# Kernel tuning notes

Hardware: AMD Instinct MI355X
Metric: run time of the kernel (lower is better)

## Reference

```python
import jax, jax.numpy as jnp
import numpy as np

D, D_SEQ, D_HEAD, N_HEAD = 256, 1280, 48, 8
N_NODE, B_GRAPH, S_LEN = 2048, 8, 1024
HDH = N_HEAD * D_HEAD  # 384
SCALE = float(np.sqrt(D_HEAD))
LN_EPS = 1e-5


def setup_inputs() -> dict:
    key = jax.random.key(0)
    ks = jax.random.split(key, 12)
    node = jax.random.normal(ks[0], (N_NODE, D), dtype=jnp.float32)
    emb = jax.random.normal(ks[1], (B_GRAPH, S_LEN, D_SEQ), dtype=jnp.float32)
    mask = jax.random.randint(ks[2], (B_GRAPH, S_LEN), 0, 2, dtype=jnp.int32)
    batch = jnp.sort(jax.random.randint(ks[3], (N_NODE,), 0, B_GRAPH, dtype=jnp.int64))
    def lin(k, fan_in, fan_out):
        lim = 1.0 / np.sqrt(fan_in)
        return jax.random.uniform(k, (fan_in, fan_out), jnp.float32, -lim, lim)
    return {
        "node": node,
        "packed_sequence_emb": emb,
        "packed_sequence_mask": mask,
        "batch": batch,
        "ln_g": jnp.ones((D,), jnp.float32),
        "ln_b": jnp.zeros((D,), jnp.float32),
        "Wq": lin(ks[4], D, HDH),
        "Wk": lin(ks[5], D_SEQ, HDH),
        "Wv": lin(ks[6], D_SEQ, HDH),
        "Wg": lin(ks[7], D, HDH),
        "bg": jnp.zeros((HDH,), jnp.float32),
        "Wback": lin(ks[8], HDH, D),
        "bback": jnp.zeros((D,), jnp.float32),
    }


def _layernorm(x, g, b):
    mu = jnp.mean(x, axis=-1, keepdims=True)
    var = jnp.mean(jnp.square(x - mu), axis=-1, keepdims=True)
    return (x - mu) * jax.lax.rsqrt(var + LN_EPS) * g + b


def reference(node, packed_sequence_emb, packed_sequence_mask, batch,
              ln_g, ln_b, Wq, Wk, Wv, Wg, bg, Wback, bback):
    N = node.shape[0]
    y = _layernorm(node, ln_g, ln_b)                                   # [N, D]
    q = (y @ Wq).reshape(N, N_HEAD, D_HEAD)                            # [N, H, Dh]
    k = (packed_sequence_emb @ Wk).reshape(B_GRAPH, S_LEN, N_HEAD, D_HEAD)
    v = (packed_sequence_emb @ Wv).reshape(B_GRAPH, S_LEN, N_HEAD, D_HEAD)

    # scores[n, s, h] = <q[n,h], k[batch[n], s, h]> / sqrt(Dh)
    scores_all = jnp.einsum('nhd,bshd->nbsh', q, k) / SCALE            # [N, B, S, H]
    scores = jnp.take_along_axis(
        scores_all, batch[:, None, None, None].astype(jnp.int32), axis=1
    )[:, 0]                                                            # [N, S, H]

    # masked softmax over sequence axis (dim=1), mask broadcast over heads
    mask_f = packed_sequence_mask[batch].astype(scores.dtype)[:, :, None]  # [N, S, 1]
    s_max = jnp.max(jnp.where(mask_f > 0, scores, -jnp.inf), axis=1, keepdims=True)
    e = jnp.exp(scores - s_max) * mask_f
    w = e / (jnp.sum(e, axis=1, keepdims=True) + 1e-9)                 # [N, S, H]

    # out[n,h,d] = sum_s w[n,s,h] * v[batch[n], s, h, d]
    feat_all = jnp.einsum('nsh,bshd->nbhd', w, v)                      # [N, B, H, Dh]
    feat = jnp.take_along_axis(
        feat_all, batch[:, None, None, None].astype(jnp.int32), axis=1
    )[:, 0]                                                            # [N, H, Dh]

    gate = jax.nn.sigmoid(y @ Wg + bg).reshape(N, N_HEAD, D_HEAD)
    new = (gate * feat).reshape(N, HDH) @ Wback + bback
    return node + new
```

## Files before the change

kernel.cpp:

```cpp
#include <hip/hip_runtime.h>
#include <hip/hip_bf16.h>
#include <math.h>

#define D 256
#define D_SEQ 1280
#define D_HEAD 48
#define N_HEAD 8
#define HDH 384
#define N_NODE 2048
#define B_GRAPH 8
#define S_LEN 1024
#define LN_EPS 1e-5f
#define QSCALE (0.14433756729740643f * 1.4426950408889634f)
#define KVN 768
#define QGN 768
#define QROWS (N_NODE + 16)
#define TPG 40
#define NWL (TPG * 8)
#define PAD_T 164864

typedef unsigned short u16;
typedef __attribute__((ext_vector_type(8))) short short8;
typedef __attribute__((ext_vector_type(4))) short short4v;
typedef __attribute__((ext_vector_type(4))) unsigned short ushort4v;
typedef __attribute__((ext_vector_type(4))) float floatx4;

__device__ __forceinline__ u16 f2bf(float f) {
    unsigned int x = __float_as_uint(f);
    x += 0x7fff + ((x >> 16) & 1);
    return (u16)(x >> 16);
}

__device__ __forceinline__ void load_lds16(const u16* g, u16* lds) {
    __builtin_amdgcn_global_load_lds(
        (const __attribute__((address_space(1))) unsigned int*)g,
        (__attribute__((address_space(3))) unsigned int*)lds, 16, 0, 0);
}

__global__ __launch_bounds__(256)
void prep(const float* __restrict__ emb, u16* __restrict__ embb,
          const float* __restrict__ node, const float* __restrict__ ln_g,
          const float* __restrict__ ln_b, u16* __restrict__ yb,
          const float* __restrict__ Wk, const float* __restrict__ Wv,
          const float* __restrict__ Wq, const float* __restrict__ Wg,
          const float* __restrict__ Wback,
          u16* __restrict__ WT, u16* __restrict__ WT2, u16* __restrict__ WbT,
          const int* __restrict__ batch, const int* __restrict__ mask,
          int* __restrict__ ranges, int* __restrict__ wl,
          int* __restrict__ kvwl, int* __restrict__ scnt,
          u16* __restrict__ Kp, u16* __restrict__ Qb) {
    const int bx = blockIdx.x;
    const int tid = threadIdx.x;
    if (bx < 1024) {
        const int b = bx >> 7, chunk = bx & 127;
        __shared__ unsigned long long words[16];
        __shared__ int wpre[17];
        #pragma unroll
        for (int c = 0; c < 4; ++c) {
            const int s = c * 256 + tid;
            const unsigned long long bal = __ballot(mask[b * S_LEN + s] != 0);
            if ((tid & 63) == 0) words[c * 4 + (tid >> 6)] = bal;
        }
        __syncthreads();
        if (tid == 0) {
            int a = 0;
            #pragma unroll
            for (int w = 0; w < 16; ++w) { wpre[w] = a; a += __popcll(words[w]); }
            wpre[16] = a;
        }
        __syncthreads();
        const int cnt = wpre[16];
        const int ce = (cnt + 127) & ~127;
        const int r = chunk * 8 + (tid >> 5);
        const int sub = tid & 31;
        const unsigned long long w = words[r >> 6];
        const bool on = (w >> (r & 63)) & 1ull;
        if (on) {
            const int rank = wpre[r >> 6] +
                __popcll(w & ((1ull << (r & 63)) - 1ull));
            const float* src = &emb[((size_t)b * S_LEN + r) * D_SEQ];
            u16* dst = &embb[((size_t)b * S_LEN + rank) * D_SEQ];
            #pragma unroll
            for (int it = 0; it < 5; ++it) {
                const int off = it * 256 + sub * 8;
                const float4 a = *(const float4*)&src[off];
                const float4 b4 = *(const float4*)&src[off + 4];
                union { u16 u[8]; int4 v; } p;
                p.u[0]=f2bf(a.x); p.u[1]=f2bf(a.y); p.u[2]=f2bf(a.z); p.u[3]=f2bf(a.w);
                p.u[4]=f2bf(b4.x); p.u[5]=f2bf(b4.y); p.u[6]=f2bf(b4.z); p.u[7]=f2bf(b4.w);
                *(int4*)&dst[off] = p.v;
            }
        }
        const int c2 = chunk * 8 + (tid >> 5);
        if (c2 >= cnt && c2 < ce) {
            u16* dst = &embb[((size_t)b * S_LEN + c2) * D_SEQ];
            const int4 z = {0, 0, 0, 0};
            #pragma unroll
            for (int it = 0; it < 5; ++it)
                *(int4*)&dst[it * 256 + sub * 8] = z;
        }
        return;
    }
    if (bx < 3072) {
        const int n = bx - 1024, t = tid;
        float x = node[n * D + t];
        float s = x, sq = x * x;
        #pragma unroll
        for (int o = 32; o > 0; o >>= 1) {
            s  += __shfl_down(s, o);
            sq += __shfl_down(sq, o);
        }
        __shared__ float ss[4], sqs[4];
        if ((t & 63) == 0) { ss[t >> 6] = s; sqs[t >> 6] = sq; }
        __syncthreads();
        float S  = ss[0] + ss[1] + ss[2] + ss[3];
        float SQ = sqs[0] + sqs[1] + sqs[2] + sqs[3];
        float mu  = S * (1.f / D);
        float var = SQ * (1.f / D) - mu * mu;
        float inv = rsqrtf(var + LN_EPS);
        yb[n * D + t] = f2bf((x - mu) * inv * ln_g[t] + ln_b[t]);
        return;
    }
    if (bx < 4320) {
        int u = bx - 3072;
        const float* W; u16* WTo; int K, kx, ny, Ncols;
        if (u < 480)      { W = Wk;    WTo = WT;                       K = D_SEQ; Ncols = HDH; kx = u % 40; ny = u / 40; }
        else if (u < 960) { u -= 480;  W = Wv; WTo = WT + (size_t)HDH * D_SEQ; K = D_SEQ; Ncols = HDH; kx = u % 40; ny = u / 40; }
        else if (u < 1056){ u -= 960;  W = Wq; WTo = WT2;              K = D;   Ncols = HDH; kx = u % 8;  ny = u / 8; }
        else if (u < 1152){ u -= 1056; W = Wg; WTo = WT2 + (size_t)HDH * D; K = D; Ncols = HDH; kx = u % 8; ny = u / 8; }
        else              { u -= 1152; W = Wback; WTo = WbT;           K = HDH; Ncols = D;   kx = u % 12; ny = u / 12; }
        const int k0 = kx * 32, n0 = ny * 32;
        __shared__ float tile[32][33];
        const int tx = tid & 31, ty = tid >> 5;
        #pragma unroll
        for (int i = 0; i < 32; i += 8)
            tile[ty + i][tx] = W[(size_t)(k0 + ty + i) * Ncols + n0 + tx];
        __syncthreads();
        #pragma unroll
        for (int i = 0; i < 32; i += 8)
            WTo[(size_t)(n0 + ty + i) * K + k0 + tx] = f2bf(tile[tx][ty + i]);
        return;
    }
    if (bx == 4320) {
        const int t = tid;
        __shared__ int msum[8][32];
        __shared__ int mcnt[8];
        const int g = t >> 5, ii = t & 31;
        int p = 0;
        #pragma unroll
        for (int k = 0; k < 32; ++k) p += mask[g * S_LEN + k * 32 + ii];
        msum[g][ii] = p;
        if (t <= B_GRAPH) {
            int lo = 0, hi = N_NODE;
            while (lo < hi) {
                int mid = (lo + hi) >> 1;
                if (batch[mid] < t) lo = mid + 1; else hi = mid;
            }
            ranges[t] = lo;
        }
        __syncthreads();
        if (t < 8) {
            int s = 0;
            #pragma unroll
            for (int k = 0; k < 32; ++k) s += msum[t][k];
            mcnt[t] = s;
            scnt[t] = s;
        }
        __syncthreads();
        if (t < B_GRAPH) {
            const int s = ranges[t];
            const int ntile = (ranges[t + 1] - s + 15) >> 4;
            for (int i = 0; i < TPG; ++i)
                wl[i * 8 + t] = (i < ntile) ? ((t << 16) | (s + i * 16)) : -1;
            const int tc = (mcnt[t] + 127) >> 7;
            for (int i = 0; i < 8; ++i)
                kvwl[i * 8 + t] = (i < tc) ? (t * S_LEN + i * 128) : -1;
        }
        return;
    }
    const int t = (bx - 4321) * 256 + tid;
    const int4 z = {0, 0, 0, 0};
    if (t < 131072) {
        const int row = t >> 1, half = t & 1;
        *(int4*)&Kp[(size_t)row * 64 + 48 + half * 8] = z;
    } else if (t < 164096) {
        const int u = t - 131072;
        const int row = u >> 1, half = u & 1;
        *(int4*)&Qb[(size_t)row * 64 + 48 + half * 8] = z;
    } else {
        const int u = t - 164096;
        const int row = u / 6, c = u - row * 6;
        const int hh = row >> 4, m = 2048 + (row & 15);
        *(int4*)&Qb[((size_t)hh * QROWS + m) * 64 + c * 8] = z;
    }
}

__global__ __launch_bounds__(256)
void kvqg_gemm(const u16* __restrict__ A, const u16* __restrict__ WT,
               u16* __restrict__ Kp, u16* __restrict__ V4,
               const u16* __restrict__ Ab, const u16* __restrict__ WT2,
               const float* __restrict__ bg, u16* __restrict__ Qb,
               float* __restrict__ gate, const int* __restrict__ kvwl) {
    __shared__ __align__(16) u16 As[128 * 32];
    __shared__ __align__(16) u16 Bs[64 * 32];
    const int tid = threadIdx.x;
    const int lane = tid & 63, wave = tid >> 6;
    const int wm64 = (wave >> 1) * 64, wn32 = (wave & 1) * 32;
    const int lm = lane & 15, lq = lane >> 4;

    if (blockIdx.x < 768) {
        const int xcd = blockIdx.x & 7;
        const int rr = blockIdx.x >> 3;
        const int nti = rr % 12;
        const int mthi = rr / 12;
        const int e = kvwl[mthi * 8 + xcd];
        if (e < 0) return;
        const int m0 = e;
        const int n0 = nti * 64;

        floatx4 acc[4][2] = {};

        const int srow = lane >> 2, scol = (lane & 3) * 8;
        const u16* ag  = &A[(size_t)(m0 + wave * 16 + srow) * D_SEQ + scol];
        const u16* ag2 = ag + (size_t)64 * D_SEQ;
        const u16* bgp = &WT[(size_t)(n0 + wave * 16 + srow) * D_SEQ + scol];
        u16* asb  = &As[wave * 512];
        u16* asb2 = &As[2048 + wave * 512];
        u16* bsb  = &Bs[wave * 512];

        for (int k0 = 0; k0 < D_SEQ; k0 += 32) {
            __syncthreads();
            load_lds16(ag + k0, asb);
            load_lds16(ag2 + k0, asb2);
            load_lds16(bgp + k0, bsb);
            __syncthreads();

            short8 af[4], bfr[2];
            #pragma unroll
            for (int i = 0; i < 4; ++i)
                af[i] = *(const short8*)&As[(wm64 + i * 16 + lm) * 32 + lq * 8];
            #pragma unroll
            for (int j = 0; j < 2; ++j)
                bfr[j] = *(const short8*)&Bs[(wn32 + j * 16 + lm) * 32 + lq * 8];
            #pragma unroll
            for (int i = 0; i < 4; ++i)
                #pragma unroll
                for (int j = 0; j < 2; ++j)
                    acc[i][j] = __builtin_amdgcn_mfma_f32_16x16x32_bf16(
                        af[i], bfr[j], acc[i][j], 0, 0, 0);
        }

        #pragma unroll
        for (int i = 0; i < 4; ++i) {
            const int mrow = m0 + wm64 + i * 16 + lq * 4;
            const int bb = mrow >> 10, s = mrow & 1023;
            #pragma unroll
            for (int j = 0; j < 2; ++j) {
                const int n = n0 + wn32 + j * 16 + lm;
                if (n < HDH) {
                    const int hh = n / 48, dd = n - hh * 48;
                    u16* kp = &Kp[(((size_t)(bb * N_HEAD + hh)) * S_LEN + s) * 64 + dd];
                    kp[0]   = f2bf(acc[i][j][0]);
                    kp[64]  = f2bf(acc[i][j][1]);
                    kp[128] = f2bf(acc[i][j][2]);
                    kp[192] = f2bf(acc[i][j][3]);
                } else {
                    const int nv = n - HDH;
                    const int hh = nv / 48, dd = nv - hh * 48;
                    ushort4v pk;
                    pk[0] = f2bf(acc[i][j][0]); pk[1] = f2bf(acc[i][j][1]);
                    pk[2] = f2bf(acc[i][j][2]); pk[3] = f2bf(acc[i][j][3]);
                    *(ushort4v*)&V4[(((size_t)(bb * N_HEAD + hh)) * (S_LEN / 4) + (s >> 2)) * 192 + dd * 4] = pk;
                }
            }
        }
        return;
    }

    {
        const int u = blockIdx.x - 768;
        const int xcd = u & 7;
        const int rr = u >> 3;
        const int nti = rr % 12;
        const int mthi = rr / 12;
        const int m0 = (mthi * 8 + xcd) * 128;
        const int n0 = nti * 64;

        floatx4 acc[4][2] = {};
        const int sr = tid >> 2;
        const int sc = (tid & 3) * 8;

        for (int k0 = 0; k0 < D; k0 += 32) {
            const int4 a0 = *(const int4*)&Ab[(size_t)(m0 + sr) * D + k0 + sc];
            const int4 a1 = *(const int4*)&Ab[(size_t)(m0 + sr + 64) * D + k0 + sc];
            const int4 b0 = *(const int4*)&WT2[(size_t)(n0 + sr) * D + k0 + sc];
            __syncthreads();
            *(int4*)&As[sr * 32 + sc] = a0;
            *(int4*)&As[(sr + 64) * 32 + sc] = a1;
            *(int4*)&Bs[sr * 32 + sc] = b0;
            __syncthreads();

            short8 af[4], bfr[2];
            #pragma unroll
            for (int i = 0; i < 4; ++i)
                af[i] = *(const short8*)&As[(wm64 + i * 16 + lm) * 32 + lq * 8];
            #pragma unroll
            for (int j = 0; j < 2; ++j)
                bfr[j] = *(const short8*)&Bs[(wn32 + j * 16 + lm) * 32 + lq * 8];
            #pragma unroll
            for (int i = 0; i < 4; ++i)
                #pragma unroll
                for (int j = 0; j < 2; ++j)
                    acc[i][j] = __builtin_amdgcn_mfma_f32_16x16x32_bf16(
                        af[i], bfr[j], acc[i][j], 0, 0, 0);
        }

        #pragma unroll
        for (int i = 0; i < 4; ++i) {
            const int mb = m0 + wm64 + i * 16 + lq * 4;
            #pragma unroll
            for (int j = 0; j < 2; ++j) {
                const int n = n0 + wn32 + j * 16 + lm;
                #pragma unroll
                for (int r = 0; r < 4; ++r) {
                    const int m = mb + r;
                    const float v = acc[i][j][r];
                    if (n < HDH) {
                        const int hh = n / 48, dd = n - hh * 48;
                        Qb[((size_t)hh * QROWS + m) * 64 + dd] = f2bf(v * QSCALE);
                    } else {
                        const int ng = n - HDH;
                        gate[(size_t)m * HDH + ng] = 1.f / (1.f + __expf(-(v + bg[ng])));
                    }
                }
            }
        }
    }
}

__global__ __launch_bounds__(256)
void back_gemm(const u16* __restrict__ Ab, const u16* __restrict__ Bt,
               const float* __restrict__ bias, const float* __restrict__ resid,
               float* __restrict__ C) {
    __shared__ __align__(16) u16 As[128 * 32];
    __shared__ __align__(16) u16 Bs[64 * 32];
    const int tid = threadIdx.x;
    const int lane = tid & 63, wave = tid >> 6;
    const int wm = (wave >> 1) * 64, wn = (wave & 1) * 32;
    const int m0 = blockIdx.y * 128, n0 = blockIdx.x * 64;
    const int lm = lane & 15, lq = lane >> 4;

    floatx4 acc[4][2] = {};
    const int sr = tid >> 2;
    const int sc = (tid & 3) * 8;

    for (int k0 = 0; k0 < HDH; k0 += 32) {
        const int4 a0 = *(const int4*)&Ab[(size_t)(m0 + sr) * HDH + k0 + sc];
        const int4 a1 = *(const int4*)&Ab[(size_t)(m0 + sr + 64) * HDH + k0 + sc];
        const int4 b0 = *(const int4*)&Bt[(size_t)(n0 + sr) * HDH + k0 + sc];
        __syncthreads();
        *(int4*)&As[sr * 32 + sc] = a0;
        *(int4*)&As[(sr + 64) * 32 + sc] = a1;
        *(int4*)&Bs[sr * 32 + sc] = b0;
        __syncthreads();

        short8 af[4], bfr[2];
        #pragma unroll
        for (int i = 0; i < 4; ++i)
            af[i] = *(const short8*)&As[(wm + i * 16 + lm) * 32 + lq * 8];
        #pragma unroll
        for (int j = 0; j < 2; ++j)
            bfr[j] = *(const short8*)&Bs[(wn + j * 16 + lm) * 32 + lq * 8];
        #pragma unroll
        for (int i = 0; i < 4; ++i)
            #pragma unroll
            for (int j = 0; j < 2; ++j)
                acc[i][j] = __builtin_amdgcn_mfma_f32_16x16x32_bf16(
                    af[i], bfr[j], acc[i][j], 0, 0, 0);
    }

    #pragma unroll
    for (int i = 0; i < 4; ++i) {
        const int mb = m0 + wm + i * 16 + lq * 4;
        #pragma unroll
        for (int j = 0; j < 2; ++j) {
            const int n = n0 + wn + j * 16 + lm;
            #pragma unroll
            for (int r = 0; r < 4; ++r) {
                const int m = mb + r;
                C[(size_t)m * D + n] = acc[i][j][r] + bias[n] + resid[(size_t)m * D + n];
            }
        }
    }
}

struct Pref {
    short8 k0, k1;
    short4v v0, v1, v2;
};

__device__ __forceinline__ Pref ldpref(const u16* kbase, const u16* vbase,
                                       int s, int lm, int lq) {
    Pref p;
    const u16* kr = &kbase[(size_t)(s + lm) * 64];
    p.k0 = *(const short8*)&kr[lq * 8];
    p.k1 = *(const short8*)&kr[32 + lq * 8];
    const size_t vo = (size_t)((s >> 2) + lq) * 192;
    p.v0 = *(const short4v*)&vbase[vo];
    p.v1 = *(const short4v*)&vbase[vo + 64];
    p.v2 = *(const short4v*)&vbase[vo + 128];
    return p;
}

__global__ __launch_bounds__(256)
void attn_mfma(const u16* __restrict__ Qb, const u16* __restrict__ Kp,
               const u16* __restrict__ V4, const int* __restrict__ scnt,
               const int* __restrict__ ranges, const int* __restrict__ wl,
               const float* __restrict__ gate, u16* __restrict__ gfeatb) {
    const int e = wl[blockIdx.x];
    if (e < 0) return;
    const int b = e >> 16, n0 = e & 0xffff;
    const int h = blockIdx.y;
    const int nend = ranges[b + 1];
    const int NT = min(16, nend - n0);

    const int tid = threadIdx.x;
    const int wave = tid >> 6, lane = tid & 63;
    const int lm = lane & 15, lq = lane >> 4;
    const int bh = b * N_HEAD + h;

    const u16* qrow = &Qb[((size_t)h * QROWS + n0 + lm) * 64];
    const short8 qf0 = *(const short8*)&qrow[lq * 8];
    const short8 qf1 = *(const short8*)&qrow[32 + lq * 8];

    const u16* kbase = &Kp[(size_t)bh * S_LEN * 64];
    const u16* vbase = &V4[(size_t)bh * (S_LEN / 4) * 192 + (size_t)lm * 4];

    const int cnt = scnt[b];
    const int T = (cnt + 15) >> 4;
    const int j = wave;
    const int nt = (j < T) ? (((T - 1 - j) >> 2) + 1) : 0;

    float l_i = 0.f;
    floatx4 acc0 = {}, acc1 = {}, acc2 = {};

    Pref pA, pB;
    if (nt > 0) pA = ldpref(kbase, vbase, j * 16, lm, lq);
    if (nt > 1) pB = ldpref(kbase, vbase, (j + 4) * 16, lm, lq);

    int t = 0;
    auto step = [&](Pref& P) {
        const int s0 = (j + t * 4) * 16;
        floatx4 st = {};
        st = __builtin_amdgcn_mfma_f32_16x16x32_bf16(P.k0, qf0, st, 0, 0, 0);
        st = __builtin_amdgcn_mfma_f32_16x16x32_bf16(P.k1, qf1, st, 0, 0, 0);
        const short4v v0 = P.v0, v1 = P.v1, v2 = P.v2;
        if (t + 2 < nt) P = ldpref(kbase, vbase, (j + (t + 2) * 4) * 16, lm, lq);

        const int rem = cnt - s0 - lq * 4;
        const float p0 = rem > 0 ? exp2f(st[0]) : 0.f;
        const float p1 = rem > 1 ? exp2f(st[1]) : 0.f;
        const float p2 = rem > 2 ? exp2f(st[2]) : 0.f;
        const float p3 = rem > 3 ? exp2f(st[3]) : 0.f;
        l_i += (p0 + p1) + (p2 + p3);

        union { __hip_bfloat162 h2[2]; short4v v; } pu;
        pu.h2[0] = __float22bfloat162_rn(make_float2(p0, p1));
        pu.h2[1] = __float22bfloat162_rn(make_float2(p2, p3));

        acc0 = __builtin_amdgcn_mfma_f32_16x16x16bf16_1k(v0, pu.v, acc0, 0, 0, 0);
        acc1 = __builtin_amdgcn_mfma_f32_16x16x16bf16_1k(v1, pu.v, acc1, 0, 0, 0);
        acc2 = __builtin_amdgcn_mfma_f32_16x16x16bf16_1k(v2, pu.v, acc2, 0, 0, 0);
        ++t;
    };
    while (t < nt) {
        step(pA);
        if (t < nt) step(pB);
    }

    l_i += __shfl_xor(l_i, 16);
    l_i += __shfl_xor(l_i, 32);

    __shared__ float sl[4][64];
    __shared__ float sacc[4][3][4][64];
    sl[wave][lane] = l_i;
    #pragma unroll
    for (int r = 0; r < 4; ++r) {
        sacc[wave][0][r][lane] = acc0[r];
        sacc[wave][1][r][lane] = acc1[r];
        sacc[wave][2][r][lane] = acc2[r];
    }
    __syncthreads();
    if (wave < 3 && lm < NT) {
        const int dt = wave;
        const float L = sl[0][lane] + sl[1][lane] + sl[2][lane] + sl[3][lane];
        const float inv = 1.f / (L + 1e-9f);
        const size_t o = (size_t)(n0 + lm) * HDH + h * 48 + dt * 16 + lq * 4;
        const float4 g = *(const float4*)&gate[o];
        float4 ov;
        ov.x = sacc[0][dt][0][lane] + sacc[1][dt][0][lane] +
               sacc[2][dt][0][lane] + sacc[3][dt][0][lane];
        ov.y = sacc[0][dt][1][lane] + sacc[1][dt][1][lane] +
               sacc[2][dt][1][lane] + sacc[3][dt][1][lane];
        ov.z = sacc[0][dt][2][lane] + sacc[1][dt][2][lane] +
               sacc[2][dt][2][lane] + sacc[3][dt][2][lane];
        ov.w = sacc[0][dt][3][lane] + sacc[1][dt][3][lane] +
               sacc[2][dt][3][lane] + sacc[3][dt][3][lane];
        union { __hip_bfloat162 h2[2]; ushort4v v; } r2;
        r2.h2[0] = __float22bfloat162_rn(make_float2(ov.x * inv * g.x,
                                                     ov.y * inv * g.y));
        r2.h2[1] = __float22bfloat162_rn(make_float2(ov.z * inv * g.z,
                                                     ov.w * inv * g.w));
        *(ushort4v*)&gfeatb[o] = r2.v;
    }
}

extern "C" void kernel_launch(void* const* d_in, const int* in_sizes, int n_in,
                              void* d_out, int out_size, void* d_ws, size_t ws_size,
                              hipStream_t stream) {
    const float* node  = (const float*)d_in[0];
    const float* emb   = (const float*)d_in[1];
    const int*   mask  = (const int*)d_in[2];
    const int*   batch = (const int*)d_in[3];
    const float* ln_g  = (const float*)d_in[4];
    const float* ln_b  = (const float*)d_in[5];
    const float* Wq    = (const float*)d_in[6];
    const float* Wk    = (const float*)d_in[7];
    const float* Wv    = (const float*)d_in[8];
    const float* Wg    = (const float*)d_in[9];
    const float* bg    = (const float*)d_in[10];
    const float* Wback = (const float*)d_in[11];
    const float* bback = (const float*)d_in[12];
    float* out = (float*)d_out;

    float* ws    = (float*)d_ws;
    float* gate  = ws;
    float* Pacc  = gate + (size_t)N_NODE * HDH;
    float* Pl    = Pacc + (size_t)2 * N_NODE * HDH;
    u16*   gfeatb = (u16*)(Pl + (size_t)2 * N_NODE * N_HEAD);
    u16*   yb    = gfeatb + (size_t)N_NODE * HDH;
    u16*   WT    = yb + (size_t)N_NODE * D;
    u16*   WT2   = WT + (size_t)KVN * D_SEQ;
    u16*   WbT   = WT2 + (size_t)QGN * D;
    u16*   Qb    = WbT + (size_t)D * HDH;
    u16*   Kp    = Qb + (size_t)N_HEAD * QROWS * 64;
    u16*   V4    = Kp + (size_t)B_GRAPH * N_HEAD * S_LEN * 64;
    u16*   embb  = V4 + (size_t)B_GRAPH * N_HEAD * (S_LEN / 4) * 192;
    int*   ranges = (int*)(embb + (size_t)B_GRAPH * S_LEN * D_SEQ);
    int*   wl    = ranges + 16;
    int*   kvwl  = wl + NWL;
    int*   scnt  = kvwl + 64;

    prep<<<4321 + PAD_T / 256, 256, 0, stream>>>(
        emb, embb, node, ln_g, ln_b, yb, Wk, Wv, Wq, Wg, Wback,
        WT, WT2, WbT, batch, mask, ranges, wl, kvwl, scnt, Kp, Qb);
    kvqg_gemm<<<960, 256, 0, stream>>>(embb, WT, Kp, V4, yb, WT2, bg, Qb, gate, kvwl);
    attn_mfma<<<dim3(NWL, N_HEAD), 256, 0, stream>>>(
        Qb, Kp, V4, scnt, ranges, wl, gate, gfeatb);
    back_gemm<<<dim3(D / 64, N_NODE / 128), 256, 0, stream>>>(
        gfeatb, WbT, bback, node, out);
}
```

Measured before the change: 166.7 us.

## Double GEMM K-step to 64 with XOR-swizzled LDS tiles and direct LDS loads

The K/V GEMM branch and the back-projection GEMM now stage 64-wide K slices instead of 32, which halves the number of barrier pairs per tile. Global rows are written into LDS with an XOR column swizzle, and fragment reads use the matching swizzle to avoid bank conflicts on the wider 128-byte rows. back_gemm switches from register-staged global loads to the direct global-to-LDS load helper. LDS use per block doubles, which may lower occupancy.

```diff
diff --git a/kernel.cpp b/kernel.cpp
--- a/kernel.cpp
+++ b/kernel.cpp
@@ -201,12 +201,16 @@
                const u16* __restrict__ Ab, const u16* __restrict__ WT2,
                const float* __restrict__ bg, u16* __restrict__ Qb,
                float* __restrict__ gate, const int* __restrict__ kvwl) {
-    __shared__ __align__(16) u16 As[128 * 32];
-    __shared__ __align__(16) u16 Bs[64 * 32];
+    __shared__ __align__(16) u16 As[128 * 64];
+    __shared__ __align__(16) u16 Bs[64 * 64];
     const int tid = threadIdx.x;
     const int lane = tid & 63, wave = tid >> 6;
     const int wm64 = (wave >> 1) * 64, wn32 = (wave & 1) * 32;
     const int lm = lane & 15, lq = lane >> 4;
+    const int r8 = lane >> 3;
+    const int csw = ((lane & 7) ^ (r8 & 7)) * 8;
+    const int s0 = (lq ^ (lm & 7)) * 8;
+    const int s1 = s0 ^ 32;
 
     if (blockIdx.x < 768) {
         const int xcd = blockIdx.x & 7;
@@ -220,34 +224,42 @@
 
         floatx4 acc[4][2] = {};
 
-        const int srow = lane >> 2, scol = (lane & 3) * 8;
-        const u16* ag  = &A[(size_t)(m0 + wave * 16 + srow) * D_SEQ + scol];
-        const u16* ag2 = ag + (size_t)64 * D_SEQ;
-        const u16* bgp = &WT[(size_t)(n0 + wave * 16 + srow) * D_SEQ + scol];
-        u16* asb  = &As[wave * 512];
-        u16* asb2 = &As[2048 + wave * 512];
-        u16* bsb  = &Bs[wave * 512];
-
-        for (int k0 = 0; k0 < D_SEQ; k0 += 32) {
+        const u16* ag  = &A[(size_t)(m0 + wave * 32 + r8) * D_SEQ + csw];
+        const u16* bgp = &WT[(size_t)(n0 + wave * 16 + r8) * D_SEQ + csw];
+
+        for (int k0 = 0; k0 < D_SEQ; k0 += 64) {
             __syncthreads();
-            load_lds16(ag + k0, asb);
-            load_lds16(ag2 + k0, asb2);
-            load_lds16(bgp + k0, bsb);
+            #pragma unroll
+            for (int it = 0; it < 4; ++it)
+                load_lds16(ag + (size_t)(it * 8) * D_SEQ + k0,
+                           &As[(wave * 32 + it * 8) * 64]);
+            #pragma unroll
+            for (int it = 0; it < 2; ++it)
+                load_lds16(bgp + (size_t)(it * 8) * D_SEQ + k0,
+                           &Bs[(wave * 16 + it * 8) * 64]);
             __syncthreads();
 
-            short8 af[4], bfr[2];
-            #pragma unroll
-            for (int i = 0; i < 4; ++i)
-                af[i] = *(const short8*)&As[(wm64 + i * 16 + lm) * 32 + lq * 8];
-            #pragma unroll
-            for (int j = 0; j < 2; ++j)
-                bfr[j] = *(const short8*)&Bs[(wn32 + j * 16 + lm) * 32 + lq * 8];
-            #pragma unroll
-            for (int i = 0; i < 4; ++i)
+            short8 af[4][2], bfv[2][2];
+            #pragma unroll
+            for (int i = 0; i < 4; ++i) {
+                const int R = wm64 + i * 16 + lm;
+                af[i][0] = *(const short8*)&As[R * 64 + s0];
+                af[i][1] = *(const short8*)&As[R * 64 + s1];
+            }
+            #pragma unroll
+            for (int j = 0; j < 2; ++j) {
+                const int R = wn32 + j * 16 + lm;
+                bfv[j][0] = *(const short8*)&Bs[R * 64 + s0];
+                bfv[j][1] = *(const short8*)&Bs[R * 64 + s1];
+            }
+            #pragma unroll
+            for (int h = 0; h < 2; ++h)
                 #pragma unroll
-                for (int j = 0; j < 2; ++j)
-                    acc[i][j] = __builtin_amdgcn_mfma_f32_16x16x32_bf16(
-                        af[i], bfr[j], acc[i][j], 0, 0, 0);
+                for (int i = 0; i < 4; ++i)
+                    #pragma unroll
+                    for (int j = 0; j < 2; ++j)
+                        acc[i][j] = __builtin_amdgcn_mfma_f32_16x16x32_bf16(
+                            af[i][h], bfv[j][h], acc[i][j], 0, 0, 0);
         }
 
         #pragma unroll
@@ -342,41 +354,56 @@
 void back_gemm(const u16* __restrict__ Ab, const u16* __restrict__ Bt,
                const float* __restrict__ bias, const float* __restrict__ resid,
                float* __restrict__ C) {
-    __shared__ __align__(16) u16 As[128 * 32];
-    __shared__ __align__(16) u16 Bs[64 * 32];
+    __shared__ __align__(16) u16 As[128 * 64];
+    __shared__ __align__(16) u16 Bs[64 * 64];
     const int tid = threadIdx.x;
     const int lane = tid & 63, wave = tid >> 6;
     const int wm = (wave >> 1) * 64, wn = (wave & 1) * 32;
     const int m0 = blockIdx.y * 128, n0 = blockIdx.x * 64;
     const int lm = lane & 15, lq = lane >> 4;
+    const int r8 = lane >> 3;
+    const int csw = ((lane & 7) ^ (r8 & 7)) * 8;
+    const int s0 = (lq ^ (lm & 7)) * 8;
+    const int s1 = s0 ^ 32;
 
     floatx4 acc[4][2] = {};
-    const int sr = tid >> 2;
-    const int sc = (tid & 3) * 8;
-
-    for (int k0 = 0; k0 < HDH; k0 += 32) {
-        const int4 a0 = *(const int4*)&Ab[(size_t)(m0 + sr) * HDH + k0 + sc];
-        const int4 a1 = *(const int4*)&Ab[(size_t)(m0 + sr + 64) * HDH + k0 + sc];
-        const int4 b0 = *(const int4*)&Bt[(size_t)(n0 + sr) * HDH + k0 + sc];
-        __syncthreads();
-        *(int4*)&As[sr * 32 + sc] = a0;
-        *(int4*)&As[(sr + 64) * 32 + sc] = a1;
-        *(int4*)&Bs[sr * 32 + sc] = b0;
-        __syncthreads();
-
-        short8 af[4], bfr[2];
-        #pragma unroll
-        for (int i = 0; i < 4; ++i)
-            af[i] = *(const short8*)&As[(wm + i * 16 + lm) * 32 + lq * 8];
-        #pragma unroll
-        for (int j = 0; j < 2; ++j)
-            bfr[j] = *(const short8*)&Bs[(wn + j * 16 + lm) * 32 + lq * 8];
-        #pragma unroll
-        for (int i = 0; i < 4; ++i)
-            #pragma unroll
-            for (int j = 0; j < 2; ++j)
-                acc[i][j] = __builtin_amdgcn_mfma_f32_16x16x32_bf16(
-                    af[i], bfr[j], acc[i][j], 0, 0, 0);
+
+    const u16* ag  = &Ab[(size_t)(m0 + wave * 32 + r8) * HDH + csw];
+    const u16* bgp = &Bt[(size_t)(n0 + wave * 16 + r8) * HDH + csw];
+
+    for (int k0 = 0; k0 < HDH; k0 += 64) {
+        __syncthreads();
+        #pragma unroll
+        for (int it = 0; it < 4; ++it)
+            load_lds16(ag + (size_t)(it * 8) * HDH + k0,
+                       &As[(wave * 32 + it * 8) * 64]);
+        #pragma unroll
+        for (int it = 0; it < 2; ++it)
+            load_lds16(bgp + (size_t)(it * 8) * HDH + k0,
+                       &Bs[(wave * 16 + it * 8) * 64]);
+        __syncthreads();
+
+        short8 af[4][2], bfv[2][2];
+        #pragma unroll
+        for (int i = 0; i < 4; ++i) {
+            const int R = wm + i * 16 + lm;
+            af[i][0] = *(const short8*)&As[R * 64 + s0];
+            af[i][1] = *(const short8*)&As[R * 64 + s1];
+        }
+        #pragma unroll
+        for (int j = 0; j < 2; ++j) {
+            const int R = wn + j * 16 + lm;
+            bfv[j][0] = *(const short8*)&Bs[R * 64 + s0];
+            bfv[j][1] = *(const short8*)&Bs[R * 64 + s1];
+        }
+        #pragma unroll
+        for (int h = 0; h < 2; ++h)
+            #pragma unroll
+            for (int i = 0; i < 4; ++i)
+                #pragma unroll
+                for (int j = 0; j < 2; ++j)
+                    acc[i][j] = __builtin_amdgcn_mfma_f32_16x16x32_bf16(
+                        af[i][h], bfv[j][h], acc[i][j], 0, 0, 0);
     }
 
     #pragma unroll
```

Result: faster. 154.0 us, median of 2 (-7.6%).
